# Optimization experiments

Hardware: AMD Instinct MI355X
Metric: run time of the kernel (lower is better)

## Reference

```python
import jax, jax.numpy as jnp
import numpy as np

VOCAB = 32000
FEAT = 1024
B, T = 16, 256


def setup_inputs() -> dict:
    key = jax.random.key(0)
    ks = jax.random.split(key, 12)
    s_in = 1.0 / np.sqrt(FEAT)
    inp = {
        "x": jax.random.randint(ks[0], (B, T), 0, VOCAB),
        "h0": jnp.zeros((2, B, FEAT), jnp.float32),
        "emb": jax.random.normal(ks[1], (VOCAB, FEAT), jnp.float32) * 0.02,
        "W_ih0": jax.random.uniform(ks[2], (3 * FEAT, FEAT), jnp.float32, -s_in, s_in),
        "W_hh0": jax.random.uniform(ks[3], (3 * FEAT, FEAT), jnp.float32, -s_in, s_in),
        "b_ih0": jax.random.uniform(ks[4], (3 * FEAT,), jnp.float32, -s_in, s_in),
        "b_hh0": jax.random.uniform(ks[5], (3 * FEAT,), jnp.float32, -s_in, s_in),
        "W_ih1": jax.random.uniform(ks[6], (3 * FEAT, FEAT), jnp.float32, -s_in, s_in),
        "W_hh1": jax.random.uniform(ks[7], (3 * FEAT, FEAT), jnp.float32, -s_in, s_in),
        "b_ih1": jax.random.uniform(ks[8], (3 * FEAT,), jnp.float32, -s_in, s_in),
        "b_hh1": jax.random.uniform(ks[9], (3 * FEAT,), jnp.float32, -s_in, s_in),
        "dec_b": jnp.zeros((VOCAB,), jnp.float32),
    }
    return inp


def _gru_layer(xs, h0, W_ih, W_hh, b_ih, b_hh):
    # xs: [T, B, H_in]; h0: [B, H]. PyTorch gate order: r, z, n.
    x_proj = jnp.einsum('tbi,gi->tbg', xs, W_ih) + b_ih  # [T, B, 3H]

    def step(h, xp):
        hp = h @ W_hh.T + b_hh  # [B, 3H]
        xr, xz, xn = jnp.split(xp, 3, axis=-1)
        hr, hz, hn = jnp.split(hp, 3, axis=-1)
        r = jax.nn.sigmoid(xr + hr)
        z = jax.nn.sigmoid(xz + hz)
        n = jnp.tanh(xn + r * hn)
        h_new = (1.0 - z) * n + z * h
        return h_new, h_new

    h_last, ys = jax.lax.scan(step, h0, x_proj)
    return ys, h_last


def reference(x, h0, emb, W_ih0, W_hh0, b_ih0, b_hh0, W_ih1, W_hh1, b_ih1, b_hh1, dec_b):
    xs = emb[x]  # [B, T, H]
    xs = jnp.transpose(xs, (1, 0, 2))  # time-major [T, B, H]
    ys0, h_last0 = _gru_layer(xs, h0[0], W_ih0, W_hh0, b_ih0, b_hh0)
    ys1, h_last1 = _gru_layer(ys0, h0[1], W_ih1, W_hh1, b_ih1, b_hh1)
    out = jnp.transpose(ys1, (1, 0, 2))  # [B, T, H]
    logits = jnp.einsum('bth,vh->btv', out, emb) + dec_b  # tied decoder
    hidden = jnp.stack([h_last0, h_last1], axis=0)  # [2, B, H]
    return logits, hidden
```

## Files before the change

kernel.cpp:

```cpp
#include <hip/hip_runtime.h>
#include <math.h>

#define FEAT 1024
#define NB 16
#define NT 256
#define VOCAB 32000
#define G3 3072
#define NWG 256
#define FLAG_STRIDE 32

#define BK 32
#define LDH 40

typedef float f4 __attribute__((ext_vector_type(4)));
typedef float f32x4 __attribute__((ext_vector_type(4)));
typedef _Float16 half4v __attribute__((ext_vector_type(4)));
typedef _Float16 half8v __attribute__((ext_vector_type(8)));

__global__ __launch_bounds__(256) void gather_kernel(const int* __restrict__ x,
                                                     const float* __restrict__ emb,
                                                     float* __restrict__ xs) {
    int row = blockIdx.x;
    int t = row >> 4;
    int b = row & 15;
    int tok = x[b * NT + t];
    const float4* src = (const float4*)(emb + (size_t)tok * FEAT);
    float4* dst = (float4*)(xs + (size_t)row * FEAT);
    dst[threadIdx.x] = src[threadIdx.x];
}

__global__ __launch_bounds__(256, 2) void gemm_split16(
        const float* __restrict__ A, const float* __restrict__ Bm,
        const float* __restrict__ bias, float* __restrict__ C,
        int M, int N, int K, int GM, int perm) {
    __shared__ _Float16 AhS[128 * LDH];
    __shared__ _Float16 AlS[128 * LDH];
    __shared__ _Float16 BhS[128 * LDH];
    __shared__ _Float16 BlS[128 * LDH];

    int nNt = N >> 7;
    int perGroup = GM * nNt;
    int g = blockIdx.x / perGroup;
    int rix = blockIdx.x % perGroup;
    int n_t = rix / GM;
    int m_t = g * GM + (rix % GM);

    int tid = threadIdx.x;
    int srow = tid >> 1;
    int shf = tid & 1;

    const float* aptr = A + (size_t)(m_t * 128 + srow) * K + shf * 16;
    const float* bptr = Bm + (size_t)(n_t * 128 + srow) * K + shf * 16;

    int wid = tid >> 6;
    int wr = wid >> 1, wc = wid & 1;
    int lane = tid & 63;
    int fr = lane & 15;
    int ke = lane >> 4;

    f32x4 acc[4][4];
#pragma unroll
    for (int i = 0; i < 4; i++)
#pragma unroll
        for (int j = 0; j < 4; j++) acc[i][j] = (f32x4){0.f, 0.f, 0.f, 0.f};

    float4 a4[4], b4[4];
#pragma unroll
    for (int q = 0; q < 4; q++) {
        a4[q] = *(const float4*)(aptr + q * 4);
        b4[q] = *(const float4*)(bptr + q * 4);
    }

    for (int k0 = 0; k0 < K; k0 += BK) {
        __syncthreads();
#pragma unroll
        for (int q = 0; q < 4; q++) {
            half4v hh, hl;
            hh.x = (_Float16)a4[q].x; hl.x = (_Float16)(a4[q].x - (float)hh.x);
            hh.y = (_Float16)a4[q].y; hl.y = (_Float16)(a4[q].y - (float)hh.y);
            hh.z = (_Float16)a4[q].z; hl.z = (_Float16)(a4[q].z - (float)hh.z);
            hh.w = (_Float16)a4[q].w; hl.w = (_Float16)(a4[q].w - (float)hh.w);
            int o = srow * LDH + shf * 16 + q * 4;
            *(half4v*)&AhS[o] = hh;
            *(half4v*)&AlS[o] = hl;
            half4v gh, gl;
            gh.x = (_Float16)b4[q].x; gl.x = (_Float16)(b4[q].x - (float)gh.x);
            gh.y = (_Float16)b4[q].y; gl.y = (_Float16)(b4[q].y - (float)gh.y);
            gh.z = (_Float16)b4[q].z; gl.z = (_Float16)(b4[q].z - (float)gh.z);
            gh.w = (_Float16)b4[q].w; gl.w = (_Float16)(b4[q].w - (float)gh.w);
            *(half4v*)&BhS[o] = gh;
            *(half4v*)&BlS[o] = gl;
        }
        __syncthreads();

        if (k0 + BK < K) {
#pragma unroll
            for (int q = 0; q < 4; q++) {
                a4[q] = *(const float4*)(aptr + k0 + BK + q * 4);
                b4[q] = *(const float4*)(bptr + k0 + BK + q * 4);
            }
        }

        half8v ah[4], al[4], bh[4], bl[4];
#pragma unroll
        for (int i = 0; i < 4; i++) {
            int ao = (wr * 64 + i * 16 + fr) * LDH + ke * 8;
            ah[i] = *(const half8v*)&AhS[ao];
            al[i] = *(const half8v*)&AlS[ao];
            int bo = (wc * 64 + i * 16 + fr) * LDH + ke * 8;
            bh[i] = *(const half8v*)&BhS[bo];
            bl[i] = *(const half8v*)&BlS[bo];
        }
#pragma unroll
        for (int i = 0; i < 4; i++)
#pragma unroll
            for (int j = 0; j < 4; j++) {
                acc[i][j] = __builtin_amdgcn_mfma_f32_16x16x32_f16(ah[i], bh[j], acc[i][j], 0, 0, 0);
                acc[i][j] = __builtin_amdgcn_mfma_f32_16x16x32_f16(ah[i], bl[j], acc[i][j], 0, 0, 0);
                acc[i][j] = __builtin_amdgcn_mfma_f32_16x16x32_f16(al[i], bh[j], acc[i][j], 0, 0, 0);
            }
    }

#pragma unroll
    for (int j = 0; j < 4; j++) {
        int col = n_t * 128 + wc * 64 + j * 16 + fr;
        float bv = bias[col];
#pragma unroll
        for (int i = 0; i < 4; i++) {
#pragma unroll
            for (int v = 0; v < 4; v++) {
                int mrow = m_t * 128 + wr * 64 + i * 16 + 4 * ke + v;
                int orow = perm ? (((mrow & 15) << 8) | (mrow >> 4)) : mrow;
                C[(size_t)orow * N + col] = acc[i][j][v] + bv;
            }
        }
    }
}

__device__ __forceinline__ void store_f32_sc(float* p, float v) {
    asm volatile("global_store_dword %0, %1, off sc0 sc1" :: "v"(p), "v"(v) : "memory");
}

__device__ __forceinline__ void grid_barrier4(unsigned* __restrict__ flags,
                                              unsigned* __restrict__ gen,
                                              unsigned expected, int bid, int tid) {
    __syncthreads();
    if (tid == 0) {
        __hip_atomic_store(&flags[bid * FLAG_STRIDE], expected,
                           __ATOMIC_RELAXED, __HIP_MEMORY_SCOPE_AGENT);
    }
    if (bid == 0) {
        unsigned v; int spins = 0;
        do {
            v = __hip_atomic_load(&flags[tid * FLAG_STRIDE],
                                  __ATOMIC_RELAXED, __HIP_MEMORY_SCOPE_AGENT);
        } while (v < expected && ++spins < (1 << 18));
        __syncthreads();
        if (tid == 0) {
            __hip_atomic_store(gen, expected,
                               __ATOMIC_RELAXED, __HIP_MEMORY_SCOPE_AGENT);
        }
    } else {
        if (tid == 0) {
            unsigned v; int spins = 0;
            do {
                v = __hip_atomic_load(gen, __ATOMIC_RELAXED,
                                      __HIP_MEMORY_SCOPE_AGENT);
                if (v >= expected) break;
                __builtin_amdgcn_s_sleep(1);
            } while (++spins < (1 << 18));
        }
    }
    __syncthreads();
}

__global__ __launch_bounds__(256, 1) void gru_scan(const float* __restrict__ xp,
                                                   const float* __restrict__ Whh,
                                                   const float* __restrict__ bhh,
                                                   const float* __restrict__ h0src,
                                                   float* __restrict__ ys,
                                                   float* __restrict__ buf0,
                                                   float* __restrict__ buf1,
                                                   float* __restrict__ hid,
                                                   unsigned* __restrict__ flags,
                                                   unsigned* __restrict__ gen,
                                                   unsigned gen_base) {
    __shared__ float w_lds[12 * 1028];
    __shared__ float red[16 * 200];
    __shared__ float sum_lds[192];
    __shared__ float bhh_lds[12];

    int wg = blockIdx.x;
    int j0 = wg * 4;
    int tid = threadIdx.x;

    for (int rr = 0; rr < 12; rr++) {
        int gate = rr >> 2, jloc = rr & 3;
        int grow = gate * FEAT + j0 + jloc;
        float4 v = ((const float4*)(Whh + (size_t)grow * FEAT))[tid];
        *(float4*)(w_lds + rr * 1028 + tid * 4) = v;
    }
    if (tid < 12) {
        int gate = tid >> 2, jloc = tid & 3;
        bhh_lds[tid] = bhh[gate * FEAT + j0 + jloc];
    }
    __syncthreads();

    int b  = tid >> 4;
    int kc = tid & 15;
    int pb = tid >> 2, pjl = tid & 3, pj = j0 + pjl;

    for (int t = 0; t < NT; t++) {
        const float* hc = (t == 0) ? h0src : ((t & 1) ? buf0 : buf1);
        float* hn = (t & 1) ? buf1 : buf0;

        float xr = 0.f, xz = 0.f, xn = 0.f;
        float hold;
        if (tid < 64) {
            const float* xpr = xp + (size_t)(t * NB + pb) * G3;
            xr = xpr[pj];
            xz = xpr[FEAT + pj];
            xn = xpr[2 * FEAT + pj];
            asm volatile("global_load_dword %0, %1, off sc0 sc1"
                         : "=&v"(hold) : "v"(hc + pb * FEAT + pj) : "memory");
        }

        f4 h4[16];
        {
            const float* hptr = hc + b * FEAT + kc * 4;
            asm volatile(
                "global_load_dwordx4 %0,  %16, off sc0 sc1\n\t"
                "global_load_dwordx4 %1,  %16, off offset:256 sc0 sc1\n\t"
                "global_load_dwordx4 %2,  %16, off offset:512 sc0 sc1\n\t"
                "global_load_dwordx4 %3,  %16, off offset:768 sc0 sc1\n\t"
                "global_load_dwordx4 %4,  %16, off offset:1024 sc0 sc1\n\t"
                "global_load_dwordx4 %5,  %16, off offset:1280 sc0 sc1\n\t"
                "global_load_dwordx4 %6,  %16, off offset:1536 sc0 sc1\n\t"
                "global_load_dwordx4 %7,  %16, off offset:1792 sc0 sc1\n\t"
                "global_load_dwordx4 %8,  %16, off offset:2048 sc0 sc1\n\t"
                "global_load_dwordx4 %9,  %16, off offset:2304 sc0 sc1\n\t"
                "global_load_dwordx4 %10, %16, off offset:2560 sc0 sc1\n\t"
                "global_load_dwordx4 %11, %16, off offset:2816 sc0 sc1\n\t"
                "global_load_dwordx4 %12, %16, off offset:3072 sc0 sc1\n\t"
                "global_load_dwordx4 %13, %16, off offset:3328 sc0 sc1\n\t"
                "global_load_dwordx4 %14, %16, off offset:3584 sc0 sc1\n\t"
                "global_load_dwordx4 %15, %16, off offset:3840 sc0 sc1\n\t"
                "s_waitcnt vmcnt(0)"
                : "=&v"(h4[0]), "=&v"(h4[1]), "=&v"(h4[2]), "=&v"(h4[3]),
                  "=&v"(h4[4]), "=&v"(h4[5]), "=&v"(h4[6]), "=&v"(h4[7]),
                  "=&v"(h4[8]), "=&v"(h4[9]), "=&v"(h4[10]), "=&v"(h4[11]),
                  "=&v"(h4[12]), "=&v"(h4[13]), "=&v"(h4[14]), "=&v"(h4[15])
                : "v"(hptr) : "memory");
            __builtin_amdgcn_sched_barrier(0);
        }

        float part[12];
#pragma unroll
        for (int rr = 0; rr < 12; rr++) part[rr] = 0.f;
#pragma unroll
        for (int q = 0; q < 16; q++) {
            int kof = q * 64 + kc * 4;
#pragma unroll
            for (int rr = 0; rr < 12; rr++) {
                f4 w = *(const f4*)&w_lds[rr * 1028 + kof];
                part[rr] = fmaf(h4[q].x, w.x, part[rr]);
                part[rr] = fmaf(h4[q].y, w.y, part[rr]);
                part[rr] = fmaf(h4[q].z, w.z, part[rr]);
                part[rr] = fmaf(h4[q].w, w.w, part[rr]);
            }
        }
#pragma unroll
        for (int rr = 0; rr < 12; rr++)
            red[kc * 200 + rr * 16 + b] = part[rr];

        asm volatile("s_waitcnt vmcnt(0)" ::: "memory");
        __builtin_amdgcn_sched_barrier(0);
        __syncthreads();

        if (tid < 192) {
            float s = 0.f;
#pragma unroll
            for (int q = 0; q < 16; q++) s += red[q * 200 + tid];
            sum_lds[tid] = s;
        }
        __syncthreads();

        if (tid < 64) {
            float dr = sum_lds[pjl * 16 + pb] + bhh_lds[pjl];
            float dz = sum_lds[(4 + pjl) * 16 + pb] + bhh_lds[4 + pjl];
            float dn = sum_lds[(8 + pjl) * 16 + pb] + bhh_lds[8 + pjl];
            float r = 1.f / (1.f + expf(-(xr + dr)));
            float z = 1.f / (1.f + expf(-(xz + dz)));
            float n = tanhf(xn + r * dn);
            float hv = (1.f - z) * n + z * hold;
            store_f32_sc(hn + pb * FEAT + pj, hv);
            ys[(size_t)(t * NB + pb) * FEAT + pj] = hv;
            if (t == NT - 1) hid[pb * FEAT + pj] = hv;
        }
        grid_barrier4(flags, gen, gen_base + t + 1, wg, tid);
    }
}

extern "C" void kernel_launch(void* const* d_in, const int* in_sizes, int n_in,
                              void* d_out, int out_size, void* d_ws, size_t ws_size,
                              hipStream_t stream) {
    const int*   x     = (const int*)d_in[0];
    const float* h0    = (const float*)d_in[1];
    const float* emb   = (const float*)d_in[2];
    const float* W_ih0 = (const float*)d_in[3];
    const float* W_hh0 = (const float*)d_in[4];
    const float* b_ih0 = (const float*)d_in[5];
    const float* b_hh0 = (const float*)d_in[6];
    const float* W_ih1 = (const float*)d_in[7];
    const float* W_hh1 = (const float*)d_in[8];
    const float* b_ih1 = (const float*)d_in[9];
    const float* b_hh1 = (const float*)d_in[10];
    const float* dec_b = (const float*)d_in[11];

    float* out = (float*)d_out;
    float* hid_out = out + (size_t)NB * NT * VOCAB;

    float* ws  = (float*)d_ws;
    float* xp  = ws;
    float* xs  = xp + (size_t)4096 * 3072;
    float* ys0 = xs + (size_t)4096 * 1024;
    float* ha  = ys0 + (size_t)4096 * 1024;
    float* hb  = ha + NB * FEAT;
    unsigned* flags = (unsigned*)(hb + NB * FEAT);
    unsigned* gen   = flags + NWG * FLAG_STRIDE;
    float* ys1 = xs;

    hipMemsetAsync((void*)flags, 0, (NWG * FLAG_STRIDE + 1) * sizeof(unsigned), stream);

    gather_kernel<<<dim3(NT * NB), dim3(256), 0, stream>>>(x, emb, xs);

    gemm_split16<<<dim3((4096 / 128) * (G3 / 128)), dim3(256), 0, stream>>>(
        xs, W_ih0, b_ih0, xp, 4096, G3, FEAT, 8, 0);

    gru_scan<<<dim3(NWG), dim3(256), 0, stream>>>(
        xp, W_hh0, b_hh0, h0, ys0, ha, hb, hid_out, flags, gen, 0u);

    gemm_split16<<<dim3((4096 / 128) * (G3 / 128)), dim3(256), 0, stream>>>(
        ys0, W_ih1, b_ih1, xp, 4096, G3, FEAT, 8, 0);

    gru_scan<<<dim3(NWG), dim3(256), 0, stream>>>(
        xp, W_hh1, b_hh1, h0 + NB * FEAT, ys1, ha, hb, hid_out + NB * FEAT,
        flags, gen, (unsigned)NT);

    gemm_split16<<<dim3((4096 / 128) * (VOCAB / 128)), dim3(256), 0, stream>>>(
        ys1, emb, dec_b, out, 4096, VOCAB, FEAT, 8, 1);
}
```

Baseline: 3.887 ms.

## Replace master-based grid barrier with all-poll packed flags and retile GRU matvec

Replaces the two-level grid barrier, where block 0 gathers strided flags and broadcasts a generation counter, with densely packed per-workgroup flags that every block polls directly using 64 threads each reading a dwordx4. This removes one hop of latency per timestep. It also retiles the recurrent matvec so each thread handles 4 batches over a 64-way K split, reusing each LDS weight load across 4 batches, with a wider padded reduction buffer. The x-projection loads for the next step are prefetched after the current step's update. The risks are more polling traffic on the flag lines, more registers, and a longer LDS reduction.

```diff
diff --git a/kernel.cpp b/kernel.cpp
--- a/kernel.cpp
+++ b/kernel.cpp
@@ -7,13 +7,13 @@
 #define VOCAB 32000
 #define G3 3072
 #define NWG 256
-#define FLAG_STRIDE 32
 
 #define BK 32
 #define LDH 40
 
 typedef float f4 __attribute__((ext_vector_type(4)));
 typedef float f32x4 __attribute__((ext_vector_type(4)));
+typedef unsigned u4 __attribute__((ext_vector_type(4)));
 typedef _Float16 half4v __attribute__((ext_vector_type(4)));
 typedef _Float16 half8v __attribute__((ext_vector_type(8)));
 
@@ -141,39 +141,6 @@
     asm volatile("global_store_dword %0, %1, off sc0 sc1" :: "v"(p), "v"(v) : "memory");
 }
 
-__device__ __forceinline__ void grid_barrier4(unsigned* __restrict__ flags,
-                                              unsigned* __restrict__ gen,
-                                              unsigned expected, int bid, int tid) {
-    __syncthreads();
-    if (tid == 0) {
-        __hip_atomic_store(&flags[bid * FLAG_STRIDE], expected,
-                           __ATOMIC_RELAXED, __HIP_MEMORY_SCOPE_AGENT);
-    }
-    if (bid == 0) {
-        unsigned v; int spins = 0;
-        do {
-            v = __hip_atomic_load(&flags[tid * FLAG_STRIDE],
-                                  __ATOMIC_RELAXED, __HIP_MEMORY_SCOPE_AGENT);
-        } while (v < expected && ++spins < (1 << 18));
-        __syncthreads();
-        if (tid == 0) {
-            __hip_atomic_store(gen, expected,
-                               __ATOMIC_RELAXED, __HIP_MEMORY_SCOPE_AGENT);
-        }
-    } else {
-        if (tid == 0) {
-            unsigned v; int spins = 0;
-            do {
-                v = __hip_atomic_load(gen, __ATOMIC_RELAXED,
-                                      __HIP_MEMORY_SCOPE_AGENT);
-                if (v >= expected) break;
-                __builtin_amdgcn_s_sleep(1);
-            } while (++spins < (1 << 18));
-        }
-    }
-    __syncthreads();
-}
-
 __global__ __launch_bounds__(256, 1) void gru_scan(const float* __restrict__ xp,
                                                    const float* __restrict__ Whh,
                                                    const float* __restrict__ bhh,
@@ -183,10 +150,9 @@
                                                    float* __restrict__ buf1,
                                                    float* __restrict__ hid,
                                                    unsigned* __restrict__ flags,
-                                                   unsigned* __restrict__ gen,
                                                    unsigned gen_base) {
     __shared__ float w_lds[12 * 1028];
-    __shared__ float red[16 * 200];
+    __shared__ float red[192 * 65];
     __shared__ float sum_lds[192];
     __shared__ float bhh_lds[12];
 
@@ -206,81 +172,87 @@
     }
     __syncthreads();
 
-    int b  = tid >> 4;
-    int kc = tid & 15;
+    int bg = tid >> 6;
+    int kc = tid & 63;
     int pb = tid >> 2, pjl = tid & 3, pj = j0 + pjl;
+
+    float xr = 0.f, xz = 0.f, xnv = 0.f;
+    if (tid < 64) {
+        const float* xpr = xp + (size_t)(0 * NB + pb) * G3;
+        xr = xpr[pj]; xz = xpr[FEAT + pj]; xnv = xpr[2 * FEAT + pj];
+    }
 
     for (int t = 0; t < NT; t++) {
         const float* hc = (t == 0) ? h0src : ((t & 1) ? buf0 : buf1);
         float* hn = (t & 1) ? buf1 : buf0;
 
-        float xr = 0.f, xz = 0.f, xn = 0.f;
-        float hold;
+        float hold = 0.f;
         if (tid < 64) {
-            const float* xpr = xp + (size_t)(t * NB + pb) * G3;
-            xr = xpr[pj];
-            xz = xpr[FEAT + pj];
-            xn = xpr[2 * FEAT + pj];
             asm volatile("global_load_dword %0, %1, off sc0 sc1"
                          : "=&v"(hold) : "v"(hc + pb * FEAT + pj) : "memory");
         }
 
         f4 h4[16];
         {
-            const float* hptr = hc + b * FEAT + kc * 4;
+            const float* p0 = hc + (bg * 4 + 0) * FEAT + kc * 4;
+            const float* p1 = hc + (bg * 4 + 1) * FEAT + kc * 4;
+            const float* p2 = hc + (bg * 4 + 2) * FEAT + kc * 4;
+            const float* p3 = hc + (bg * 4 + 3) * FEAT + kc * 4;
             asm volatile(
                 "global_load_dwordx4 %0,  %16, off sc0 sc1\n\t"
-                "global_load_dwordx4 %1,  %16, off offset:256 sc0 sc1\n\t"
-                "global_load_dwordx4 %2,  %16, off offset:512 sc0 sc1\n\t"
-                "global_load_dwordx4 %3,  %16, off offset:768 sc0 sc1\n\t"
-                "global_load_dwordx4 %4,  %16, off offset:1024 sc0 sc1\n\t"
-                "global_load_dwordx4 %5,  %16, off offset:1280 sc0 sc1\n\t"
-                "global_load_dwordx4 %6,  %16, off offset:1536 sc0 sc1\n\t"
-                "global_load_dwordx4 %7,  %16, off offset:1792 sc0 sc1\n\t"
-                "global_load_dwordx4 %8,  %16, off offset:2048 sc0 sc1\n\t"
-                "global_load_dwordx4 %9,  %16, off offset:2304 sc0 sc1\n\t"
-                "global_load_dwordx4 %10, %16, off offset:2560 sc0 sc1\n\t"
-                "global_load_dwordx4 %11, %16, off offset:2816 sc0 sc1\n\t"
-                "global_load_dwordx4 %12, %16, off offset:3072 sc0 sc1\n\t"
-                "global_load_dwordx4 %13, %16, off offset:3328 sc0 sc1\n\t"
-                "global_load_dwordx4 %14, %16, off offset:3584 sc0 sc1\n\t"
-                "global_load_dwordx4 %15, %16, off offset:3840 sc0 sc1\n\t"
+                "global_load_dwordx4 %1,  %16, off offset:1024 sc0 sc1\n\t"
+                "global_load_dwordx4 %2,  %16, off offset:2048 sc0 sc1\n\t"
+                "global_load_dwordx4 %3,  %16, off offset:3072 sc0 sc1\n\t"
+                "global_load_dwordx4 %4,  %17, off sc0 sc1\n\t"
+                "global_load_dwordx4 %5,  %17, off offset:1024 sc0 sc1\n\t"
+                "global_load_dwordx4 %6,  %17, off offset:2048 sc0 sc1\n\t"
+                "global_load_dwordx4 %7,  %17, off offset:3072 sc0 sc1\n\t"
+                "global_load_dwordx4 %8,  %18, off sc0 sc1\n\t"
+                "global_load_dwordx4 %9,  %18, off offset:1024 sc0 sc1\n\t"
+                "global_load_dwordx4 %10, %18, off offset:2048 sc0 sc1\n\t"
+                "global_load_dwordx4 %11, %18, off offset:3072 sc0 sc1\n\t"
+                "global_load_dwordx4 %12, %19, off sc0 sc1\n\t"
+                "global_load_dwordx4 %13, %19, off offset:1024 sc0 sc1\n\t"
+                "global_load_dwordx4 %14, %19, off offset:2048 sc0 sc1\n\t"
+                "global_load_dwordx4 %15, %19, off offset:3072 sc0 sc1\n\t"
                 "s_waitcnt vmcnt(0)"
                 : "=&v"(h4[0]), "=&v"(h4[1]), "=&v"(h4[2]), "=&v"(h4[3]),
                   "=&v"(h4[4]), "=&v"(h4[5]), "=&v"(h4[6]), "=&v"(h4[7]),
                   "=&v"(h4[8]), "=&v"(h4[9]), "=&v"(h4[10]), "=&v"(h4[11]),
                   "=&v"(h4[12]), "=&v"(h4[13]), "=&v"(h4[14]), "=&v"(h4[15])
-                : "v"(hptr) : "memory");
+                : "v"(p0), "v"(p1), "v"(p2), "v"(p3) : "memory");
             __builtin_amdgcn_sched_barrier(0);
         }
 
-        float part[12];
-#pragma unroll
-        for (int rr = 0; rr < 12; rr++) part[rr] = 0.f;
-#pragma unroll
-        for (int q = 0; q < 16; q++) {
-            int kof = q * 64 + kc * 4;
+        float part[48];
+#pragma unroll
+        for (int i = 0; i < 48; i++) part[i] = 0.f;
+#pragma unroll
+        for (int q = 0; q < 4; q++) {
+            int kof = q * 256 + kc * 4;
 #pragma unroll
             for (int rr = 0; rr < 12; rr++) {
                 f4 w = *(const f4*)&w_lds[rr * 1028 + kof];
-                part[rr] = fmaf(h4[q].x, w.x, part[rr]);
-                part[rr] = fmaf(h4[q].y, w.y, part[rr]);
-                part[rr] = fmaf(h4[q].z, w.z, part[rr]);
-                part[rr] = fmaf(h4[q].w, w.w, part[rr]);
+#pragma unroll
+                for (int bi = 0; bi < 4; bi++) {
+                    part[rr * 4 + bi] = fmaf(h4[bi * 4 + q].x, w.x, part[rr * 4 + bi]);
+                    part[rr * 4 + bi] = fmaf(h4[bi * 4 + q].y, w.y, part[rr * 4 + bi]);
+                    part[rr * 4 + bi] = fmaf(h4[bi * 4 + q].z, w.z, part[rr * 4 + bi]);
+                    part[rr * 4 + bi] = fmaf(h4[bi * 4 + q].w, w.w, part[rr * 4 + bi]);
+                }
             }
         }
 #pragma unroll
         for (int rr = 0; rr < 12; rr++)
-            red[kc * 200 + rr * 16 + b] = part[rr];
-
-        asm volatile("s_waitcnt vmcnt(0)" ::: "memory");
-        __builtin_amdgcn_sched_barrier(0);
+#pragma unroll
+            for (int bi = 0; bi < 4; bi++)
+                red[(rr * 16 + bg * 4 + bi) * 65 + kc] = part[rr * 4 + bi];
         __syncthreads();
 
         if (tid < 192) {
             float s = 0.f;
 #pragma unroll
-            for (int q = 0; q < 16; q++) s += red[q * 200 + tid];
+            for (int q = 0; q < 64; q++) s += red[tid * 65 + q];
             sum_lds[tid] = s;
         }
         __syncthreads();
@@ -291,13 +263,37 @@
             float dn = sum_lds[(8 + pjl) * 16 + pb] + bhh_lds[8 + pjl];
             float r = 1.f / (1.f + expf(-(xr + dr)));
             float z = 1.f / (1.f + expf(-(xz + dz)));
-            float n = tanhf(xn + r * dn);
+            float n = tanhf(xnv + r * dn);
             float hv = (1.f - z) * n + z * hold;
             store_f32_sc(hn + pb * FEAT + pj, hv);
             ys[(size_t)(t * NB + pb) * FEAT + pj] = hv;
             if (t == NT - 1) hid[pb * FEAT + pj] = hv;
-        }
-        grid_barrier4(flags, gen, gen_base + t + 1, wg, tid);
+            int tn = (t + 1 < NT) ? t + 1 : t;
+            const float* xpr = xp + (size_t)(tn * NB + pb) * G3;
+            xr = xpr[pj]; xz = xpr[FEAT + pj]; xnv = xpr[2 * FEAT + pj];
+        }
+
+        __syncthreads();
+        unsigned expected = gen_base + t + 1;
+        if (tid == 0) {
+            asm volatile("s_waitcnt vmcnt(0)\n\t"
+                         "global_store_dword %0, %1, off sc0 sc1"
+                         :: "v"(&flags[wg]), "v"(expected) : "memory");
+        }
+        {
+            const unsigned* fp = flags + 4 * (tid & 63);
+            u4 v; int spins = 0;
+            while (true) {
+                asm volatile("global_load_dwordx4 %0, %1, off sc0 sc1\n\t"
+                             "s_waitcnt vmcnt(0)"
+                             : "=&v"(v) : "v"(fp) : "memory");
+                if (v.x >= expected && v.y >= expected &&
+                    v.z >= expected && v.w >= expected) break;
+                if (++spins > (1 << 20)) break;
+                __builtin_amdgcn_s_sleep(1);
+            }
+            __builtin_amdgcn_sched_barrier(0);
+        }
     }
 }
 
@@ -327,10 +323,9 @@
     float* ha  = ys0 + (size_t)4096 * 1024;
     float* hb  = ha + NB * FEAT;
     unsigned* flags = (unsigned*)(hb + NB * FEAT);
-    unsigned* gen   = flags + NWG * FLAG_STRIDE;
     float* ys1 = xs;
 
-    hipMemsetAsync((void*)flags, 0, (NWG * FLAG_STRIDE + 1) * sizeof(unsigned), stream);
+    hipMemsetAsync((void*)flags, 0, 512 * sizeof(unsigned), stream);
 
     gather_kernel<<<dim3(NT * NB), dim3(256), 0, stream>>>(x, emb, xs);
 
@@ -338,14 +333,14 @@
         xs, W_ih0, b_ih0, xp, 4096, G3, FEAT, 8, 0);
 
     gru_scan<<<dim3(NWG), dim3(256), 0, stream>>>(
-        xp, W_hh0, b_hh0, h0, ys0, ha, hb, hid_out, flags, gen, 0u);
+        xp, W_hh0, b_hh0, h0, ys0, ha, hb, hid_out, flags, 0u);
 
     gemm_split16<<<dim3((4096 / 128) * (G3 / 128)), dim3(256), 0, stream>>>(
         ys0, W_ih1, b_ih1, xp, 4096, G3, FEAT, 8, 0);
 
     gru_scan<<<dim3(NWG), dim3(256), 0, stream>>>(
         xp, W_hh1, b_hh1, h0 + NB * FEAT, ys1, ha, hb, hid_out + NB * FEAT,
-        flags, gen, (unsigned)NT);
+        flags, (unsigned)NT);
 
     gemm_split16<<<dim3((4096 / 128) * (VOCAB / 128)), dim3(256), 0, stream>>>(
         ys1, emb, dec_b, out, 4096, VOCAB, FEAT, 8, 1);
```

Result: slower. 4.836 ms (+24.4%).
